# Kernel optimization log

Measured on AMD Instinct MI355X. Metric: run time of the kernel, lower is better.

Reference implementation:

```python
import jax, jax.numpy as jnp
import numpy as np

ROUTINGS = 3

def squash(t, axis=-1):
    s2 = jnp.sum(jnp.square(t), axis=axis, keepdims=True)
    safe_norm = jnp.sqrt(s2 + 1e-7)
    scale = s2 / (1.0 + s2)
    return scale * (t / safe_norm)

def setup_inputs() -> dict:
    key = jax.random.key(0)
    k1, k2 = jax.random.split(key)
    B, I, K = 64, 2048, 8      # batch, input_num_caps, input_dim_caps
    J, L = 32, 16              # num_caps, dim_caps
    inputs = jax.random.normal(k1, (B, I, K), dtype=jnp.float32)
    # glorot-uniform-ish init for W [I, J, K, L]
    limit = np.sqrt(6.0 / (K + L)).astype(np.float32)
    W = jax.random.uniform(k2, (I, J, K, L), dtype=jnp.float32, minval=-limit, maxval=limit)
    return {"inputs": inputs, "W": W}

def reference(inputs, W):
    # uji: predicted capsules [B, I, J, L]
    uji = jnp.einsum('ijkl,bik->bijl', W, inputs)
    B, I, J, _ = uji.shape
    b = jnp.zeros((B, I, J, 1), dtype=uji.dtype)
    vj = None
    for _ in range(ROUTINGS):
        cj = jax.nn.softmax(b, axis=-1)          # size-1 axis -> all ones (faithful)
        s = jnp.sum(cj * uji, axis=1, keepdims=True)  # [B, 1, J, L]
        s = s[..., None]                          # [B, 1, J, L, 1]
        vj = squash(s, axis=-2)                   # squash over L
        # agreement: contract over L (k) and trailing size-1 axis (z)
        agreement = jnp.einsum('bijk,bmjkz->bijm', uji, vj)  # [B, I, J, 1]
        b = b + agreement
    return vj
```

## Files before the change

kernel.cpp:

```cpp
#include <hip/hip_runtime.h>
#include <hip/hip_bf16.h>
#include <stdint.h>


using f32x4 = __attribute__((ext_vector_type(4))) float;
using s16x4 = __attribute__((ext_vector_type(4))) short;
using s16x8 = __attribute__((ext_vector_type(8))) short;

__device__ __forceinline__ short f2bf(float x) {
    __hip_bfloat16 h = __float2bfloat16(x);
    return *reinterpret_cast<short*>(&h);
}
__device__ __forceinline__ float bf2f(short s) {
    return __uint_as_float(((uint32_t)(uint16_t)s) << 16);
}


__global__ __launch_bounds__(256)
void caps_prep(const float* __restrict__ In, float* __restrict__ ws)
{
    const int g = blockIdx.x * 256 + threadIdx.x;
    short* hi = (short*)(ws + 32768);
    short* lo = hi + (1 << 20);
    f32x4 v = *(const f32x4*)(In + (size_t)g * 4);
    s16x4 h4, l4;
    #pragma unroll
    for (int e = 0; e < 4; ++e) {
        short h = f2bf(v[e]);
        h4[e] = h;
        l4[e] = f2bf(v[e] - bf2f(h));
    }
    *(s16x4*)(hi + (size_t)g * 4) = h4;
    *(s16x4*)(lo + (size_t)g * 4) = l4;
    if (blockIdx.x < 128) ws[blockIdx.x * 256 + threadIdx.x] = 0.0f;
}

struct WReg { float v[8]; };
struct AReg { s16x8 h[4], l[4]; };

__global__ __launch_bounds__(256)
void caps_gemm_at(const float* __restrict__ W, float* __restrict__ ws)
{
    const int tid = threadIdx.x, wv = tid >> 6, lane = tid & 63;
    const int q = lane >> 4, cin = lane & 15;
    const int kb0 = blockIdx.x * 256;
    const int j   = blockIdx.y * 4 + wv;
    const short* hi = (const short*)(ws + 32768);
    const short* lo = hi + (1 << 20);
    const float* wbase = W + (size_t)j * 128 + cin;

    f32x4 acc[4] = {};

    auto load_step = [&](int s, WReg& wr, AReg& ar) {
        const int i0 = (kb0 >> 3) + s * 4 + q;
        const float* wp = wbase + (size_t)i0 * 4096;
        #pragma unroll
        for (int e = 0; e < 8; ++e) wr.v[e] = wp[e * 16];
        const int kb = kb0 + s * 32 + q * 8;
        #pragma unroll
        for (int mt = 0; mt < 4; ++mt) {
            const size_t o = (size_t)(mt * 16 + cin) * 16384 + kb;
            ar.h[mt] = *(const s16x8*)(hi + o);
            ar.l[mt] = *(const s16x8*)(lo + o);
        }
    };

    auto compute = [&](const WReg& wr, const AReg& ar) {
        s16x8 Bh, Bl;
        #pragma unroll
        for (int e = 0; e < 8; ++e) {
            short h = f2bf(wr.v[e]);
            Bh[e] = h;
            Bl[e] = f2bf(wr.v[e] - bf2f(h));
        }
        #pragma unroll
        for (int mt = 0; mt < 4; ++mt) {
            acc[mt] = __builtin_amdgcn_mfma_f32_16x16x32_bf16(ar.h[mt], Bh, acc[mt], 0, 0, 0);
            acc[mt] = __builtin_amdgcn_mfma_f32_16x16x32_bf16(ar.l[mt], Bh, acc[mt], 0, 0, 0);
            acc[mt] = __builtin_amdgcn_mfma_f32_16x16x32_bf16(ar.h[mt], Bl, acc[mt], 0, 0, 0);
        }
    };

    WReg wA, wB; AReg aA, aB;
    load_step(0, wA, aA);
    #pragma unroll 1
    for (int ss = 0; ss < 8; ss += 2) {
        load_step(ss + 1, wB, aB);
        compute(wA, aA);
        if (ss + 2 < 8) load_step(ss + 2, wA, aA);
        compute(wB, aB);
    }

    #pragma unroll
    for (int mt = 0; mt < 4; ++mt) {
        const int b = mt * 16 + q * 4;
        #pragma unroll
        for (int r = 0; r < 4; ++r)
            atomicAdd(ws + (b + r) * 512 + j * 16 + cin, acc[mt][r]);
    }
}

__global__ __launch_bounds__(256)
void caps_squash(const float* __restrict__ ws, float* __restrict__ out)
{
    const int o = blockIdx.x * 256 + threadIdx.x;
    float s = ws[o];
    float s2 = s * s;
    s2 += __shfl_xor(s2, 1);
    s2 += __shfl_xor(s2, 2);
    s2 += __shfl_xor(s2, 4);
    s2 += __shfl_xor(s2, 8);
    const float scale = s2 / (1.0f + s2);
    out[o] = s * scale / sqrtf(s2 + 1e-7f);
}

__global__ __launch_bounds__(256)
void caps_gemm_direct(const float* __restrict__ In, const float* __restrict__ W,
                      float* __restrict__ outp)
{
    const int tid = threadIdx.x, wv = tid >> 6, lane = tid & 63;
    const int q = lane >> 4, cin = lane & 15;
    const int c0 = blockIdx.y * 128 + wv * 32;
    f32x4 acc[4][2] = {};
    #pragma unroll 1
    for (int ssk = 0; ssk < 512; ++ssk) {
        const int kb = ssk * 32;
        const int i0 = (kb >> 3) + q;
        float wvv[2][8];
        s16x8 Ah[4], Al[4];
        #pragma unroll
        for (int nt = 0; nt < 2; ++nt) {
            const int c = c0 + nt * 16 + cin;
            const float* wp = W + (size_t)i0 * 4096 + (c >> 4) * 128 + (c & 15);
            #pragma unroll
            for (int e = 0; e < 8; ++e) wvv[nt][e] = wp[e * 16];
        }
        #pragma unroll
        for (int mt = 0; mt < 4; ++mt) {
            const float* ip = In + (size_t)(mt * 16 + cin) * 16384 + kb + q * 8;
            #pragma unroll
            for (int e = 0; e < 8; ++e) {
                float x = ip[e];
                short h = f2bf(x);
                Ah[mt][e] = h;
                Al[mt][e] = f2bf(x - bf2f(h));
            }
        }
        #pragma unroll
        for (int nt = 0; nt < 2; ++nt) {
            s16x8 Bh, Bl;
            #pragma unroll
            for (int e = 0; e < 8; ++e) {
                float x = wvv[nt][e];
                short h = f2bf(x);
                Bh[e] = h;
                Bl[e] = f2bf(x - bf2f(h));
            }
            #pragma unroll
            for (int mt = 0; mt < 4; ++mt) {
                acc[mt][nt] = __builtin_amdgcn_mfma_f32_16x16x32_bf16(Ah[mt], Bh, acc[mt][nt], 0, 0, 0);
                acc[mt][nt] = __builtin_amdgcn_mfma_f32_16x16x32_bf16(Al[mt], Bh, acc[mt][nt], 0, 0, 0);
                acc[mt][nt] = __builtin_amdgcn_mfma_f32_16x16x32_bf16(Ah[mt], Bl, acc[mt][nt], 0, 0, 0);
            }
        }
    }
    #pragma unroll
    for (int mt = 0; mt < 4; ++mt)
        #pragma unroll
        for (int nt = 0; nt < 2; ++nt) {
            const int c = c0 + nt * 16 + cin;
            #pragma unroll
            for (int r = 0; r < 4; ++r)
                outp[(mt * 16 + q * 4 + r) * 512 + c] = acc[mt][nt][r];
        }
}

__global__ __launch_bounds__(256)
void caps_squash_inplace(float* __restrict__ out)
{
    const int o = blockIdx.x * 256 + threadIdx.x;
    float s = out[o];
    float s2 = s * s;
    s2 += __shfl_xor(s2, 1);
    s2 += __shfl_xor(s2, 2);
    s2 += __shfl_xor(s2, 4);
    s2 += __shfl_xor(s2, 8);
    const float scale = s2 / (1.0f + s2);
    out[o] = s * scale / sqrtf(s2 + 1e-7f);
}

extern "C" void kernel_launch(void* const* d_in, const int* in_sizes, int n_in,
                              void* d_out, int out_size, void* d_ws, size_t ws_size,
                              hipStream_t stream)
{
    (void)in_sizes; (void)n_in; (void)out_size;
    const float* In = (const float*)d_in[0];
    const float* W  = (const float*)d_in[1];
    float* out = (float*)d_out;
    float* ws  = (float*)d_ws;

    const size_t need = 32768u * sizeof(float) + (2u << 20) * sizeof(short) * 2;
    if (ws_size >= need) {
        caps_prep    <<<dim3(1024),     dim3(256), 0, stream>>>(In, ws);
        caps_gemm_at <<<dim3(64, 8),    dim3(256), 0, stream>>>(W, ws);
        caps_squash  <<<dim3(128),      dim3(256), 0, stream>>>(ws, out);
    } else {
        caps_gemm_direct   <<<dim3(1, 4), dim3(256), 0, stream>>>(In, W, out);
        caps_squash_inplace<<<dim3(128),  dim3(256), 0, stream>>>(out);
    }
}
```

Measured before the change: 99.99 us.

## Fuse input bf16 split into GEMM and replace atomics with split-K partial reduction

Drops the separate prep kernel that split inputs into bf16 hi/lo arrays; the GEMM now loads fp32 inputs directly and does the hi/lo split in registers before the MFMAs. The atomicAdd accumulation is replaced by per-K-block partial sums written to workspace, which a finish kernel reduces (64 partials) before squashing. This saves one launch, the zeroing step and the atomic contention, in exchange for more conversion work inside the GEMM, more input bytes loaded, and an extra 8 MB of partial-sum traffic.

```diff
diff --git a/kernel.cpp b/kernel.cpp
--- a/kernel.cpp
+++ b/kernel.cpp
@@ -4,7 +4,6 @@
 
 
 using f32x4 = __attribute__((ext_vector_type(4))) float;
-using s16x4 = __attribute__((ext_vector_type(4))) short;
 using s16x8 = __attribute__((ext_vector_type(8))) short;
 
 __device__ __forceinline__ short f2bf(float x) {
@@ -15,43 +14,26 @@
     return __uint_as_float(((uint32_t)(uint16_t)s) << 16);
 }
 
-
-__global__ __launch_bounds__(256)
-void caps_prep(const float* __restrict__ In, float* __restrict__ ws)
-{
-    const int g = blockIdx.x * 256 + threadIdx.x;
-    short* hi = (short*)(ws + 32768);
-    short* lo = hi + (1 << 20);
-    f32x4 v = *(const f32x4*)(In + (size_t)g * 4);
-    s16x4 h4, l4;
-    #pragma unroll
-    for (int e = 0; e < 4; ++e) {
-        short h = f2bf(v[e]);
-        h4[e] = h;
-        l4[e] = f2bf(v[e] - bf2f(h));
-    }
-    *(s16x4*)(hi + (size_t)g * 4) = h4;
-    *(s16x4*)(lo + (size_t)g * 4) = l4;
-    if (blockIdx.x < 128) ws[blockIdx.x * 256 + threadIdx.x] = 0.0f;
-}
-
-struct WReg { float v[8]; };
-struct AReg { s16x8 h[4], l[4]; };
-
-__global__ __launch_bounds__(256)
-void caps_gemm_at(const float* __restrict__ W, float* __restrict__ ws)
-{
-    const int tid = threadIdx.x, wv = tid >> 6, lane = tid & 63;
-    const int q = lane >> 4, cin = lane & 15;
-    const int kb0 = blockIdx.x * 256;
-    const int j   = blockIdx.y * 4 + wv;
-    const short* hi = (const short*)(ws + 32768);
-    const short* lo = hi + (1 << 20);
+struct WReg { float v[8];    };
+struct IBuf { f32x4 v[4][2]; };
+
+__global__ __launch_bounds__(256)
+void caps_gemm(const float* __restrict__ In, const float* __restrict__ W,
+               float* __restrict__ ws)
+{
+    const int tid  = threadIdx.x;
+    const int wv   = tid >> 6;
+    const int lane = tid & 63;
+    const int q    = lane >> 4;
+    const int cin  = lane & 15;
+    const int kb0  = blockIdx.x * 256;
+    const int j    = blockIdx.y * 4 + wv;
+
     const float* wbase = W + (size_t)j * 128 + cin;
 
     f32x4 acc[4] = {};
 
-    auto load_step = [&](int s, WReg& wr, AReg& ar) {
+    auto load_step = [&](int s, WReg& wr, IBuf& ib) {
         const int i0 = (kb0 >> 3) + s * 4 + q;
         const float* wp = wbase + (size_t)i0 * 4096;
         #pragma unroll
@@ -59,13 +41,13 @@
         const int kb = kb0 + s * 32 + q * 8;
         #pragma unroll
         for (int mt = 0; mt < 4; ++mt) {
-            const size_t o = (size_t)(mt * 16 + cin) * 16384 + kb;
-            ar.h[mt] = *(const s16x8*)(hi + o);
-            ar.l[mt] = *(const s16x8*)(lo + o);
+            const float* ip = In + (size_t)(mt * 16 + cin) * 16384 + kb;
+            ib.v[mt][0] = *(const f32x4*)(ip);
+            ib.v[mt][1] = *(const f32x4*)(ip + 4);
         }
     };
 
-    auto compute = [&](const WReg& wr, const AReg& ar) {
+    auto compute = [&](const WReg& wr, const IBuf& ib) {
         s16x8 Bh, Bl;
         #pragma unroll
         for (int e = 0; e < 8; ++e) {
@@ -75,36 +57,51 @@
         }
         #pragma unroll
         for (int mt = 0; mt < 4; ++mt) {
-            acc[mt] = __builtin_amdgcn_mfma_f32_16x16x32_bf16(ar.h[mt], Bh, acc[mt], 0, 0, 0);
-            acc[mt] = __builtin_amdgcn_mfma_f32_16x16x32_bf16(ar.l[mt], Bh, acc[mt], 0, 0, 0);
-            acc[mt] = __builtin_amdgcn_mfma_f32_16x16x32_bf16(ar.h[mt], Bl, acc[mt], 0, 0, 0);
+            s16x8 Ah, Al;
+            #pragma unroll
+            for (int e = 0; e < 8; ++e) {
+                float x = ib.v[mt][e >> 2][e & 3];
+                short h = f2bf(x);
+                Ah[e] = h;
+                Al[e] = f2bf(x - bf2f(h));
+            }
+            acc[mt] = __builtin_amdgcn_mfma_f32_16x16x32_bf16(Ah, Bh, acc[mt], 0, 0, 0);
+            acc[mt] = __builtin_amdgcn_mfma_f32_16x16x32_bf16(Al, Bh, acc[mt], 0, 0, 0);
+            acc[mt] = __builtin_amdgcn_mfma_f32_16x16x32_bf16(Ah, Bl, acc[mt], 0, 0, 0);
         }
     };
 
-    WReg wA, wB; AReg aA, aB;
-    load_step(0, wA, aA);
+    WReg wA, wB; IBuf iA, iB;
+    load_step(0, wA, iA);
     #pragma unroll 1
     for (int ss = 0; ss < 8; ss += 2) {
-        load_step(ss + 1, wB, aB);
-        compute(wA, aA);
-        if (ss + 2 < 8) load_step(ss + 2, wA, aA);
-        compute(wB, aB);
-    }
-
+        load_step(ss + 1, wB, iB);
+        compute(wA, iA);
+        if (ss + 2 < 8) load_step(ss + 2, wA, iA);
+        compute(wB, iB);
+    }
+
+    float* wsb = ws + (size_t)blockIdx.x * 32768;
     #pragma unroll
     for (int mt = 0; mt < 4; ++mt) {
         const int b = mt * 16 + q * 4;
         #pragma unroll
         for (int r = 0; r < 4; ++r)
-            atomicAdd(ws + (b + r) * 512 + j * 16 + cin, acc[mt][r]);
-    }
-}
-
-__global__ __launch_bounds__(256)
-void caps_squash(const float* __restrict__ ws, float* __restrict__ out)
+            wsb[(b + r) * 512 + j * 16 + cin] = acc[mt][r];
+    }
+}
+
+__global__ __launch_bounds__(256)
+void caps_finish(const float* __restrict__ ws, float* __restrict__ out)
 {
     const int o = blockIdx.x * 256 + threadIdx.x;
-    float s = ws[o];
+    float a[8] = {};
+    #pragma unroll 1
+    for (int ks = 0; ks < 64; ks += 8)
+        #pragma unroll
+        for (int u = 0; u < 8; ++u)
+            a[u] += ws[(size_t)(ks + u) * 32768 + o];
+    float s = ((a[0] + a[1]) + (a[2] + a[3])) + ((a[4] + a[5]) + (a[6] + a[7]));
     float s2 = s * s;
     s2 += __shfl_xor(s2, 1);
     s2 += __shfl_xor(s2, 2);
@@ -199,11 +196,10 @@
     float* out = (float*)d_out;
     float* ws  = (float*)d_ws;
 
-    const size_t need = 32768u * sizeof(float) + (2u << 20) * sizeof(short) * 2;
+    const size_t need = 64u * 32768u * sizeof(float);
     if (ws_size >= need) {
-        caps_prep    <<<dim3(1024),     dim3(256), 0, stream>>>(In, ws);
-        caps_gemm_at <<<dim3(64, 8),    dim3(256), 0, stream>>>(W, ws);
-        caps_squash  <<<dim3(128),      dim3(256), 0, stream>>>(ws, out);
+        caps_gemm  <<<dim3(64, 8), dim3(256), 0, stream>>>(In, W, ws);
+        caps_finish<<<dim3(128),   dim3(256), 0, stream>>>(ws, out);
     } else {
         caps_gemm_direct   <<<dim3(1, 4), dim3(256), 0, stream>>>(In, W, out);
         caps_squash_inplace<<<dim3(128),  dim3(256), 0, stream>>>(out);
```

New measurement: 93.74 us. 1.07x faster.
